# Optimization experiments

Hardware: AMD Instinct MI355X
Metric: run time of the kernel (lower is better)

The kernel has to match this reference:

```python
import jax, jax.numpy as jnp
import numpy as np

NX, NY, NC, NT = 320, 320, 20, 25


def ifft2c(x):
    # centered orthonormal 2D inverse FFT over axes (0,1)
    return jnp.fft.fftshift(
        jnp.fft.ifft2(jnp.fft.ifftshift(x, axes=(0, 1)), axes=(0, 1), norm='ortho'),
        axes=(0, 1))


def warp_bilinear(im, flw):
    # im: [Nx,Ny] complex, flw: [Nx,Ny,2] float pixel displacements
    # Sparse motion matrix application = bilinear gather at (x+u, y+v)
    Nx, Ny = im.shape
    gx, gy = jnp.meshgrid(jnp.arange(Nx, dtype=jnp.float32),
                          jnp.arange(Ny, dtype=jnp.float32), indexing='ij')
    xs = jnp.clip(gx + flw[..., 0], 0.0, Nx - 1.0)
    ys = jnp.clip(gy + flw[..., 1], 0.0, Ny - 1.0)
    x0 = jnp.floor(xs).astype(jnp.int32)
    y0 = jnp.floor(ys).astype(jnp.int32)
    x1 = jnp.minimum(x0 + 1, Nx - 1)
    y1 = jnp.minimum(y0 + 1, Ny - 1)
    wx = xs - x0.astype(jnp.float32)
    wy = ys - y0.astype(jnp.float32)
    return (im[x0, y0] * ((1 - wx) * (1 - wy))
            + im[x1, y0] * (wx * (1 - wy))
            + im[x0, y1] * ((1 - wx) * wy)
            + im[x1, y1] * (wx * wy))


def setup_inputs() -> dict:
    key = jax.random.key(0)
    ks = jax.random.split(key, 6)
    return {
        'kspace_re': jax.random.normal(ks[0], (NX, NY, NC), dtype=jnp.float32),
        'kspace_im': jax.random.normal(ks[1], (NX, NY, NC), dtype=jnp.float32),
        'mask': jax.random.uniform(ks[2], (NX, NY, NC, NT), dtype=jnp.float32),
        'smaps_re': jax.random.normal(ks[3], (NX, NY, NC), dtype=jnp.float32),
        'smaps_im': jax.random.normal(ks[4], (NX, NY, NC), dtype=jnp.float32),
        'flow': jax.random.normal(ks[5], (NX, NY, 2, NT), dtype=jnp.float32),
    }


def reference(kspace_re, kspace_im, mask, smaps_re, smaps_im, flow):
    kspace = kspace_re + 1j * kspace_im          # [Nx,Ny,Nc]
    smaps = smaps_re + 1j * smaps_im             # [Nx,Ny,Nc]
    # masked kspace for all motion states: [Nx,Ny,Nc,Nt]
    ksp_t = kspace[..., None] * mask.astype(kspace.dtype)
    coil_ims = ifft2c(ksp_t)                     # [Nx,Ny,Nc,Nt]
    # coil combine: sum_c ifft2c(k*m) * conj(smaps) -> [Nx,Ny,Nt]
    im_t = jnp.sum(coil_ims * jnp.conj(smaps)[..., None], axis=2)
    # per-frame sparse motion warp, then sum over motion states
    warped = jax.vmap(warp_bilinear, in_axes=(2, 3))(im_t, flow)  # [Nt,Nx,Ny]
    out = jnp.sum(warped, axis=0)                # [Nx,Ny] complex
    return jnp.stack([out.real, out.imag])       # [2,Nx,Ny] float32 view
```

## Files before the change

### kernel.cpp

```cpp
#include <hip/hip_runtime.h>
#include <hip/hip_fp16.h>
#include <math.h>

#define NXY 320
#define NC 20
#define NT 25
#define NPIX 102400
#define PI_F 3.14159265358979f
#define TWOPI_F 6.28318530717959f

__device__ __forceinline__ float2 cmul(float2 a, float2 b) {
    return make_float2(a.x * b.x - a.y * b.y, a.x * b.y + a.y * b.x);
}

struct Tw {
    float2 st[6];
    float  sgn[6];
    float2 w5[5];
    int J;
};

__device__ __forceinline__ void tw_init(Tw& t) {
    const int lane = threadIdx.x & 63;
    #pragma unroll
    for (int s = 0; s < 6; ++s) {
        const int h = 32 >> s;
        const bool up = (lane & h) != 0;
        t.sgn[s] = up ? -1.0f : 1.0f;
        if (up) {
            float ss, cc;
            __sincosf(PI_F * (float)(lane & (h - 1)) / (float)h, &ss, &cc);
            t.st[s] = make_float2(cc, ss);
        } else {
            t.st[s] = make_float2(1.0f, 0.0f);
        }
    }
    t.J = (int)(__brev((unsigned)lane) >> 26);
    t.w5[0] = make_float2(1.0f, 0.0f);
    #pragma unroll
    for (int r = 1; r < 5; ++r) {
        float ss, cc;
        __sincosf(TWOPI_F * (float)(r * t.J) / 320.0f, &ss, &cc);
        t.w5[r] = make_float2(cc, ss);
    }
}

__device__ __forceinline__ void fft320(const Tw& t, float2 x[5], float2 out[5]) {
    #pragma unroll
    for (int s = 0; s < 6; ++s) {
        const int h = 32 >> s;
        #pragma unroll
        for (int r = 0; r < 5; ++r) {
            float ox = __shfl_xor(x[r].x, h);
            float oy = __shfl_xor(x[r].y, h);
            float dx = fmaf(t.sgn[s], x[r].x, ox);
            float dy = fmaf(t.sgn[s], x[r].y, oy);
            x[r].x = dx * t.st[s].x - dy * t.st[s].y;
            x[r].y = dx * t.st[s].y + dy * t.st[s].x;
        }
    }
    float2 T[5];
    T[0] = x[0];
    #pragma unroll
    for (int r = 1; r < 5; ++r) T[r] = cmul(x[r], t.w5[r]);
    const float W5x[5] = {1.0f, 0.309016994f, -0.809016994f, -0.809016994f, 0.309016994f};
    const float W5y[5] = {0.0f, 0.951056516f, 0.587785252f, -0.587785252f, -0.951056516f};
    #pragma unroll
    for (int s5 = 0; s5 < 5; ++s5) {
        float2 acc = T[0];
        #pragma unroll
        for (int r = 1; r < 5; ++r) {
            const int k = (r * s5) % 5;
            acc.x += T[r].x * W5x[k] - T[r].y * W5y[k];
            acc.y += T[r].x * W5y[k] + T[r].y * W5x[k];
        }
        out[s5] = acc;
    }
}

__global__ __launch_bounds__(256) void k_prep_smaps(const float* __restrict__ smr,
                                                    const float* __restrict__ smi,
                                                    float2* __restrict__ smapsC) {
    const int p0 = blockIdx.x * 64;
    __shared__ float s_r[64 * 21];
    __shared__ float s_i[64 * 21];
    for (int j = threadIdx.x; j < 64 * NC; j += blockDim.x) {
        int p = j / NC, c = j - p * NC;
        s_r[p * 21 + c] = smr[(size_t)p0 * NC + j];
        s_i[p * 21 + c] = smi[(size_t)p0 * NC + j];
    }
    __syncthreads();
    for (int j = threadIdx.x; j < 64 * NC; j += blockDim.x) {
        int c = j >> 6, p = j & 63;
        int pg = p0 + p;
        int m = pg / NXY, n = pg - m * NXY;
        float sgn = (((m + n) & 1) ? -1.0f : 1.0f) * (1.0f / 320.0f);
        smapsC[(size_t)c * NPIX + pg] = make_float2(s_r[p * 21 + c] * sgn,
                                                    -s_i[p * 21 + c] * sgn);
    }
}

__global__ __launch_bounds__(256) void k_perm_smaps(const float2* __restrict__ smapsC,
                                                    __half2* __restrict__ smapsP) {
    const int c = blockIdx.x;
    const int s5 = blockIdx.y;
    const int v0 = blockIdx.z * 64;
    __shared__ __half2 t2[64 * 65];
    for (int j = threadIdx.x; j < 64 * 64; j += blockDim.x) {
        int ur = j >> 6, vc = j & 63;
        float2 v = smapsC[(size_t)c * NPIX + (size_t)(s5 * 64 + ur) * NXY + v0 + vc];
        t2[ur * 65 + vc] = __floats2half2_rn(v.x, v.y);
    }
    __syncthreads();
    for (int j = threadIdx.x; j < 64 * 64; j += blockDim.x) {
        int vr = j >> 6, lane = j & 63;
        int J = (int)(__brev((unsigned)lane) >> 26);
        smapsP[(size_t)((c * NXY + v0 + vr) * 5 + s5) * 64 + lane] = t2[J * 65 + vr];
    }
}

__global__ __launch_bounds__(256) void k_prep_input(const float* __restrict__ ksr,
                                                    const float* __restrict__ ksi,
                                                    const float* __restrict__ mask,
                                                    __half2* __restrict__ X0,
                                                    int t0, int G) {
    const int Q = NC * G;
    const int QP = Q + 1;
    const int p0 = blockIdx.x * 16;
    __shared__ float s_mask[16 * 501];
    __shared__ float s_kr[16 * 21];
    __shared__ float s_ki[16 * 21];
    for (int j = threadIdx.x; j < 16 * NC; j += blockDim.x) {
        int p = j / NC, c = j - p * NC;
        s_kr[p * 21 + c] = ksr[(size_t)p0 * NC + j];
        s_ki[p * 21 + c] = ksi[(size_t)p0 * NC + j];
    }
    for (int j = threadIdx.x; j < 16 * Q; j += blockDim.x) {
        int p = j / Q, qq = j - p * Q;
        int c = qq / G, tc = qq - c * G;
        s_mask[p * QP + qq] =
            mask[(size_t)(p0 + p) * (NC * NT) + c * NT + (t0 + tc)];
    }
    __syncthreads();
    for (int j = threadIdx.x; j < 16 * Q; j += blockDim.x) {
        int p = j & 15, q = j >> 4;
        int c = q / G;
        int pg = p0 + p;
        int m = pg / NXY, n = pg - m * NXY;
        float sgn = ((m + n) & 1) ? -1.0f : 1.0f;
        float mk = s_mask[p * QP + q] * sgn;
        X0[(size_t)q * NPIX + pg] =
            __floats2half2_rn(s_kr[p * 21 + c] * mk, s_ki[p * 21 + c] * mk);
    }
}

__global__ __launch_bounds__(256) void k_fft_rows(const __half2* __restrict__ X0,
                                                  __half2* __restrict__ Z, int G) {
    const int mtile = blockIdx.x;
    const int tc = blockIdx.y;
    const int c = blockIdx.z;
    const int q = c * G + tc;
    const int wave = threadIdx.x >> 6;
    const int lane = threadIdx.x & 63;
    const int m0 = mtile * 16;
    __shared__ __half2 tile[NXY * 17];
    Tw t;
    tw_init(t);
    const __half2* src = X0 + (size_t)q * NPIX;
    #pragma unroll
    for (int rnd = 0; rnd < 4; ++rnd) {
        int mm = rnd * 4 + wave;
        const __half2* row = src + (size_t)(m0 + mm) * NXY + lane * 5;
        float2 x[5], out[5];
        #pragma unroll
        for (int r = 0; r < 5; ++r) x[r] = __half22float2(row[r]);
        fft320(t, x, out);
        #pragma unroll
        for (int s5 = 0; s5 < 5; ++s5) {
            int v = t.J + 64 * s5;
            tile[v * 17 + mm] = __floats2half2_rn(out[s5].x, out[s5].y);
        }
    }
    __syncthreads();
    __half2* dst = Z + (size_t)q * NPIX + m0;
    for (int j = threadIdx.x; j < NXY * 16; j += blockDim.x) {
        int mm = j & 15, v = j >> 4;
        dst[(size_t)v * NXY + mm] = tile[v * 17 + mm];
    }
}

__global__ __launch_bounds__(256) void k_fft_cols_combine(const __half2* __restrict__ Z,
                                                          const __half2* __restrict__ smapsP,
                                                          float2* __restrict__ imt,
                                                          int t0, int G) {
    const int vtile = blockIdx.x;
    const int tc = blockIdx.y;
    const int wave = threadIdx.x >> 6;
    const int lane = threadIdx.x & 63;
    const int v0 = vtile * 8;
    __shared__ float tile_x[NXY * 9];
    __shared__ float tile_y[NXY * 9];
    Tw t;
    tw_init(t);
    float2 accA[5], accB[5];
    #pragma unroll
    for (int s5 = 0; s5 < 5; ++s5) {
        accA[s5] = make_float2(0.f, 0.f);
        accB[s5] = make_float2(0.f, 0.f);
    }
    const int vA = v0 + wave;
    const int vB = v0 + 4 + wave;
    for (int c = 0; c < NC; ++c) {
        const __half2* zc = Z + (size_t)(c * G + tc) * NPIX;
        {
            const __half2* col = zc + (size_t)vA * NXY + lane * 5;
            float2 x[5], out[5];
            #pragma unroll
            for (int r = 0; r < 5; ++r) x[r] = __half22float2(col[r]);
            fft320(t, x, out);
            const __half2* sp = smapsP + (size_t)((c * NXY + vA) * 5) * 64 + lane;
            #pragma unroll
            for (int s5 = 0; s5 < 5; ++s5) {
                float2 sm = __half22float2(sp[s5 * 64]);
                float2 tt = cmul(out[s5], sm);
                accA[s5].x += tt.x;
                accA[s5].y += tt.y;
            }
        }
        {
            const __half2* col = zc + (size_t)vB * NXY + lane * 5;
            float2 x[5], out[5];
            #pragma unroll
            for (int r = 0; r < 5; ++r) x[r] = __half22float2(col[r]);
            fft320(t, x, out);
            const __half2* sp = smapsP + (size_t)((c * NXY + vB) * 5) * 64 + lane;
            #pragma unroll
            for (int s5 = 0; s5 < 5; ++s5) {
                float2 sm = __half22float2(sp[s5 * 64]);
                float2 tt = cmul(out[s5], sm);
                accB[s5].x += tt.x;
                accB[s5].y += tt.y;
            }
        }
    }
    #pragma unroll
    for (int s5 = 0; s5 < 5; ++s5) {
        int u = t.J + 64 * s5;
        tile_x[u * 9 + wave] = accA[s5].x;
        tile_y[u * 9 + wave] = accA[s5].y;
        tile_x[u * 9 + 4 + wave] = accB[s5].x;
        tile_y[u * 9 + 4 + wave] = accB[s5].y;
    }
    __syncthreads();
    float2* dst = imt + (size_t)(t0 + tc) * NPIX + v0;
    for (int j = threadIdx.x; j < NXY * 8; j += blockDim.x) {
        int vv = j & 7, u = j >> 3;
        dst[(size_t)u * NXY + vv] = make_float2(tile_x[u * 9 + vv], tile_y[u * 9 + vv]);
    }
}

__global__ __launch_bounds__(256) void k_warp_sum(const float2* __restrict__ imt,
                                                  const float* __restrict__ flow,
                                                  float* __restrict__ out) {
    int p = blockIdx.x * blockDim.x + threadIdx.x;
    if (p >= NPIX) return;
    int x = p / NXY, y = p - x * NXY;
    float fx = (float)x, fy = (float)y;
    float ar = 0.f, ai = 0.f;
    const float* fl = flow + (size_t)p * (2 * NT);
    for (int t = 0; t < NT; ++t) {
        float u = fl[t];
        float v = fl[NT + t];
        float xs = fminf(fmaxf(fx + u, 0.0f), 319.0f);
        float ys = fminf(fmaxf(fy + v, 0.0f), 319.0f);
        float x0f = floorf(xs), y0f = floorf(ys);
        int x0 = (int)x0f, y0 = (int)y0f;
        int x1 = min(x0 + 1, NXY - 1), y1 = min(y0 + 1, NXY - 1);
        float wx = xs - x0f, wy = ys - y0f;
        const float2* base = imt + (size_t)t * NPIX;
        float2 c00 = base[x0 * NXY + y0];
        float2 c01 = base[x0 * NXY + y1];
        float2 c10 = base[x1 * NXY + y0];
        float2 c11 = base[x1 * NXY + y1];
        float w00 = (1.f - wx) * (1.f - wy), w01 = (1.f - wx) * wy;
        float w10 = wx * (1.f - wy), w11 = wx * wy;
        ar += c00.x * w00 + c01.x * w01 + c10.x * w10 + c11.x * w11;
        ai += c00.y * w00 + c01.y * w01 + c10.y * w10 + c11.y * w11;
    }
    out[p] = ar;
    out[NPIX + p] = ai;
}

extern "C" void kernel_launch(void* const* d_in, const int* in_sizes, int n_in,
                              void* d_out, int out_size, void* d_ws, size_t ws_size,
                              hipStream_t stream) {
    const float* ksr = (const float*)d_in[0];
    const float* ksi = (const float*)d_in[1];
    const float* mask = (const float*)d_in[2];
    const float* smr = (const float*)d_in[3];
    const float* smi = (const float*)d_in[4];
    const float* flow = (const float*)d_in[5];
    float* out = (float*)d_out;

    char* ws = (char*)d_ws;
    const size_t smapsC_bytes = (size_t)NC * NPIX * sizeof(float2);
    const size_t smapsP_bytes = (size_t)NC * NPIX * 5 * 64 / NXY * sizeof(__half2);
    const size_t imt_bytes = (size_t)NT * NPIX * sizeof(float2);
    const size_t fixed = smapsC_bytes + smapsP_bytes + imt_bytes;
    const size_t per_t = (size_t)2 * NC * NPIX * sizeof(__half2);

    int G = 1;
    if (ws_size > fixed + per_t) {
        size_t g = (ws_size - fixed) / per_t;
        G = (int)(g > (size_t)NT ? (size_t)NT : g);
    }
    if (G < 1) G = 1;

    float2* smapsC = (float2*)ws;
    __half2* smapsP = (__half2*)(ws + smapsC_bytes);
    float2* imt = (float2*)(ws + smapsC_bytes + smapsP_bytes);
    __half2* X0 = (__half2*)(ws + fixed);
    __half2* Z = (__half2*)(ws + fixed + (size_t)NC * G * NPIX * sizeof(__half2));

    k_prep_smaps<<<NPIX / 64, 256, 0, stream>>>(smr, smi, smapsC);
    k_perm_smaps<<<dim3(NC, 5, 5), 256, 0, stream>>>(smapsC, smapsP);
    for (int t0 = 0; t0 < NT; t0 += G) {
        int g = (NT - t0) < G ? (NT - t0) : G;
        k_prep_input<<<NPIX / 16, 256, 0, stream>>>(ksr, ksi, mask, X0, t0, g);
        k_fft_rows<<<dim3(20, g, NC), 256, 0, stream>>>(X0, Z, g);
        k_fft_cols_combine<<<dim3(40, g), 256, 0, stream>>>(Z, smapsP, imt, t0, g);
    }
    k_warp_sum<<<(NPIX + 255) / 256, 256, 0, stream>>>(imt, flow, out);
}
```

Baseline: 902.3 us.

## Batch FFTs per wave, split coil sum across blocks, stage flow in LDS

Several changes at once. The FFT routine is templated to process K independent transforms together, so the row and column passes interleave shuffles for ILP. The column/coil-combine kernel is split into two coil halves along a new grid dimension, doubling parallelism, and each half writes its partial image in fp16. The warp kernel then sums the two partials during its gathers. Mask loading in prep_input is made contiguous, and the warp kernel stages flow through LDS with coalesced loads. The trade-offs are extra gather traffic for the two partial images, fp16 precision loss on the intermediate images, and higher register pressure from batched FFTs.

```diff
diff --git a/kernel.cpp b/kernel.cpp
--- a/kernel.cpp
+++ b/kernel.cpp
@@ -45,36 +45,43 @@
     }
 }
 
-__device__ __forceinline__ void fft320(const Tw& t, float2 x[5], float2 out[5]) {
+template <int K>
+__device__ __forceinline__ void fft320xK(const Tw& t, float2 (&x)[K][5], float2 (&out)[K][5]) {
     #pragma unroll
     for (int s = 0; s < 6; ++s) {
         const int h = 32 >> s;
         #pragma unroll
         for (int r = 0; r < 5; ++r) {
-            float ox = __shfl_xor(x[r].x, h);
-            float oy = __shfl_xor(x[r].y, h);
-            float dx = fmaf(t.sgn[s], x[r].x, ox);
-            float dy = fmaf(t.sgn[s], x[r].y, oy);
-            x[r].x = dx * t.st[s].x - dy * t.st[s].y;
-            x[r].y = dx * t.st[s].y + dy * t.st[s].x;
-        }
-    }
-    float2 T[5];
-    T[0] = x[0];
-    #pragma unroll
-    for (int r = 1; r < 5; ++r) T[r] = cmul(x[r], t.w5[r]);
+            #pragma unroll
+            for (int k = 0; k < K; ++k) {
+                float ox = __shfl_xor(x[k][r].x, h);
+                float oy = __shfl_xor(x[k][r].y, h);
+                float dx = fmaf(t.sgn[s], x[k][r].x, ox);
+                float dy = fmaf(t.sgn[s], x[k][r].y, oy);
+                x[k][r].x = dx * t.st[s].x - dy * t.st[s].y;
+                x[k][r].y = dx * t.st[s].y + dy * t.st[s].x;
+            }
+        }
+    }
     const float W5x[5] = {1.0f, 0.309016994f, -0.809016994f, -0.809016994f, 0.309016994f};
     const float W5y[5] = {0.0f, 0.951056516f, 0.587785252f, -0.587785252f, -0.951056516f};
     #pragma unroll
-    for (int s5 = 0; s5 < 5; ++s5) {
-        float2 acc = T[0];
-        #pragma unroll
-        for (int r = 1; r < 5; ++r) {
-            const int k = (r * s5) % 5;
-            acc.x += T[r].x * W5x[k] - T[r].y * W5y[k];
-            acc.y += T[r].x * W5y[k] + T[r].y * W5x[k];
-        }
-        out[s5] = acc;
+    for (int k = 0; k < K; ++k) {
+        float2 T[5];
+        T[0] = x[k][0];
+        #pragma unroll
+        for (int r = 1; r < 5; ++r) T[r] = cmul(x[k][r], t.w5[r]);
+        #pragma unroll
+        for (int s5 = 0; s5 < 5; ++s5) {
+            float2 acc = T[0];
+            #pragma unroll
+            for (int r = 1; r < 5; ++r) {
+                const int kk = (r * s5) % 5;
+                acc.x += T[r].x * W5x[kk] - T[r].y * W5y[kk];
+                acc.y += T[r].x * W5y[kk] + T[r].y * W5x[kk];
+            }
+            out[k][s5] = acc;
+        }
     }
 }
 
@@ -124,8 +131,6 @@
                                                     const float* __restrict__ mask,
                                                     __half2* __restrict__ X0,
                                                     int t0, int G) {
-    const int Q = NC * G;
-    const int QP = Q + 1;
     const int p0 = blockIdx.x * 16;
     __shared__ float s_mask[16 * 501];
     __shared__ float s_kr[16 * 21];
@@ -135,22 +140,26 @@
         s_kr[p * 21 + c] = ksr[(size_t)p0 * NC + j];
         s_ki[p * 21 + c] = ksi[(size_t)p0 * NC + j];
     }
-    for (int j = threadIdx.x; j < 16 * Q; j += blockDim.x) {
-        int p = j / Q, qq = j - p * Q;
-        int c = qq / G, tc = qq - c * G;
-        s_mask[p * QP + qq] =
-            mask[(size_t)(p0 + p) * (NC * NT) + c * NT + (t0 + tc)];
-    }
-    __syncthreads();
-    for (int j = threadIdx.x; j < 16 * Q; j += blockDim.x) {
-        int p = j & 15, q = j >> 4;
-        int c = q / G;
-        int pg = p0 + p;
-        int m = pg / NXY, n = pg - m * NXY;
-        float sgn = ((m + n) & 1) ? -1.0f : 1.0f;
-        float mk = s_mask[p * QP + q] * sgn;
-        X0[(size_t)q * NPIX + pg] =
-            __floats2half2_rn(s_kr[p * 21 + c] * mk, s_ki[p * 21 + c] * mk);
+    for (int j = threadIdx.x; j < 16 * 500; j += blockDim.x) {
+        int p = j / 500, col = j - p * 500;
+        s_mask[p * 501 + col] = mask[(size_t)p0 * 500 + j];
+    }
+    __syncthreads();
+    const int p = threadIdx.x & 15;
+    const int g16 = threadIdx.x >> 4;
+    const int pg = p0 + p;
+    const int m = pg / NXY;
+    const int n = pg - m * NXY;
+    const float sgn = ((m + n) & 1) ? -1.0f : 1.0f;
+    #pragma unroll
+    for (int c = 0; c < NC; ++c) {
+        const float kr = s_kr[p * 21 + c] * sgn;
+        const float ki = s_ki[p * 21 + c] * sgn;
+        for (int tc = g16; tc < G; tc += 16) {
+            const int q = c * G + tc;
+            const float mk = s_mask[p * 501 + c * NT + t0 + tc];
+            X0[(size_t)q * NPIX + pg] = __floats2half2_rn(kr * mk, ki * mk);
+        }
     }
 }
 
@@ -167,18 +176,21 @@
     Tw t;
     tw_init(t);
     const __half2* src = X0 + (size_t)q * NPIX;
-    #pragma unroll
-    for (int rnd = 0; rnd < 4; ++rnd) {
-        int mm = rnd * 4 + wave;
-        const __half2* row = src + (size_t)(m0 + mm) * NXY + lane * 5;
-        float2 x[5], out[5];
-        #pragma unroll
-        for (int r = 0; r < 5; ++r) x[r] = __half22float2(row[r]);
-        fft320(t, x, out);
+    float2 x[4][5], out[4][5];
+    #pragma unroll
+    for (int k = 0; k < 4; ++k) {
+        const __half2* row = src + (size_t)(m0 + wave + 4 * k) * NXY + lane * 5;
+        #pragma unroll
+        for (int r = 0; r < 5; ++r) x[k][r] = __half22float2(row[r]);
+    }
+    fft320xK<4>(t, x, out);
+    #pragma unroll
+    for (int k = 0; k < 4; ++k) {
+        const int mm = wave + 4 * k;
         #pragma unroll
         for (int s5 = 0; s5 < 5; ++s5) {
             int v = t.J + 64 * s5;
-            tile[v * 17 + mm] = __floats2half2_rn(out[s5].x, out[s5].y);
+            tile[v * 17 + mm] = __floats2half2_rn(out[k][s5].x, out[k][s5].y);
         }
     }
     __syncthreads();
@@ -191,97 +203,99 @@
 
 __global__ __launch_bounds__(256) void k_fft_cols_combine(const __half2* __restrict__ Z,
                                                           const __half2* __restrict__ smapsP,
-                                                          float2* __restrict__ imt,
+                                                          __half2* __restrict__ imtP,
                                                           int t0, int G) {
     const int vtile = blockIdx.x;
     const int tc = blockIdx.y;
+    const int half = blockIdx.z;
     const int wave = threadIdx.x >> 6;
     const int lane = threadIdx.x & 63;
     const int v0 = vtile * 8;
-    __shared__ float tile_x[NXY * 9];
-    __shared__ float tile_y[NXY * 9];
+    const int vA = v0 + wave;
+    const int vB = v0 + 4 + wave;
+    __shared__ __half2 tile[NXY * 9];
     Tw t;
     tw_init(t);
-    float2 accA[5], accB[5];
-    #pragma unroll
-    for (int s5 = 0; s5 < 5; ++s5) {
-        accA[s5] = make_float2(0.f, 0.f);
-        accB[s5] = make_float2(0.f, 0.f);
-    }
-    const int vA = v0 + wave;
-    const int vB = v0 + 4 + wave;
-    for (int c = 0; c < NC; ++c) {
+    float2 acc[2][5];
+    #pragma unroll
+    for (int k = 0; k < 2; ++k)
+        #pragma unroll
+        for (int s5 = 0; s5 < 5; ++s5) acc[k][s5] = make_float2(0.f, 0.f);
+    const int c0 = half * 10;
+    for (int c = c0; c < c0 + 10; ++c) {
         const __half2* zc = Z + (size_t)(c * G + tc) * NPIX;
-        {
-            const __half2* col = zc + (size_t)vA * NXY + lane * 5;
-            float2 x[5], out[5];
-            #pragma unroll
-            for (int r = 0; r < 5; ++r) x[r] = __half22float2(col[r]);
-            fft320(t, x, out);
-            const __half2* sp = smapsP + (size_t)((c * NXY + vA) * 5) * 64 + lane;
-            #pragma unroll
-            for (int s5 = 0; s5 < 5; ++s5) {
-                float2 sm = __half22float2(sp[s5 * 64]);
-                float2 tt = cmul(out[s5], sm);
-                accA[s5].x += tt.x;
-                accA[s5].y += tt.y;
-            }
-        }
-        {
-            const __half2* col = zc + (size_t)vB * NXY + lane * 5;
-            float2 x[5], out[5];
-            #pragma unroll
-            for (int r = 0; r < 5; ++r) x[r] = __half22float2(col[r]);
-            fft320(t, x, out);
-            const __half2* sp = smapsP + (size_t)((c * NXY + vB) * 5) * 64 + lane;
-            #pragma unroll
-            for (int s5 = 0; s5 < 5; ++s5) {
-                float2 sm = __half22float2(sp[s5 * 64]);
-                float2 tt = cmul(out[s5], sm);
-                accB[s5].x += tt.x;
-                accB[s5].y += tt.y;
-            }
+        float2 x[2][5], out[2][5];
+        const __half2* colA = zc + (size_t)vA * NXY + lane * 5;
+        const __half2* colB = zc + (size_t)vB * NXY + lane * 5;
+        #pragma unroll
+        for (int r = 0; r < 5; ++r) {
+            x[0][r] = __half22float2(colA[r]);
+            x[1][r] = __half22float2(colB[r]);
+        }
+        fft320xK<2>(t, x, out);
+        const __half2* spA = smapsP + (size_t)((c * NXY + vA) * 5) * 64 + lane;
+        const __half2* spB = smapsP + (size_t)((c * NXY + vB) * 5) * 64 + lane;
+        #pragma unroll
+        for (int s5 = 0; s5 < 5; ++s5) {
+            float2 smA = __half22float2(spA[s5 * 64]);
+            float2 smB = __half22float2(spB[s5 * 64]);
+            float2 ta = cmul(out[0][s5], smA);
+            float2 tb = cmul(out[1][s5], smB);
+            acc[0][s5].x += ta.x; acc[0][s5].y += ta.y;
+            acc[1][s5].x += tb.x; acc[1][s5].y += tb.y;
         }
     }
     #pragma unroll
     for (int s5 = 0; s5 < 5; ++s5) {
         int u = t.J + 64 * s5;
-        tile_x[u * 9 + wave] = accA[s5].x;
-        tile_y[u * 9 + wave] = accA[s5].y;
-        tile_x[u * 9 + 4 + wave] = accB[s5].x;
-        tile_y[u * 9 + 4 + wave] = accB[s5].y;
-    }
-    __syncthreads();
-    float2* dst = imt + (size_t)(t0 + tc) * NPIX + v0;
+        tile[u * 9 + wave] = __floats2half2_rn(acc[0][s5].x, acc[0][s5].y);
+        tile[u * 9 + 4 + wave] = __floats2half2_rn(acc[1][s5].x, acc[1][s5].y);
+    }
+    __syncthreads();
+    __half2* dst = imtP + (size_t)(half * NT + t0 + tc) * NPIX + v0;
     for (int j = threadIdx.x; j < NXY * 8; j += blockDim.x) {
         int vv = j & 7, u = j >> 3;
-        dst[(size_t)u * NXY + vv] = make_float2(tile_x[u * 9 + vv], tile_y[u * 9 + vv]);
-    }
-}
-
-__global__ __launch_bounds__(256) void k_warp_sum(const float2* __restrict__ imt,
+        dst[(size_t)u * NXY + vv] = tile[u * 9 + vv];
+    }
+}
+
+__global__ __launch_bounds__(256) void k_warp_sum(const __half2* __restrict__ imtP,
                                                   const float* __restrict__ flow,
                                                   float* __restrict__ out) {
-    int p = blockIdx.x * blockDim.x + threadIdx.x;
-    if (p >= NPIX) return;
-    int x = p / NXY, y = p - x * NXY;
-    float fx = (float)x, fy = (float)y;
+    const int p0 = blockIdx.x * 256;
+    const int tid = threadIdx.x;
+    __shared__ float s_fl[2 * NT * 257];
+    for (int j = tid; j < 256 * 50; j += 256) {
+        int pp = j / 50, rem = j - pp * 50;
+        int d = rem / 25, tt = rem - d * 25;
+        s_fl[(d * NT + tt) * 257 + pp] = flow[(size_t)p0 * 50 + j];
+    }
+    __syncthreads();
+    const int p = p0 + tid;
+    const int x = p / NXY, y = p - x * NXY;
+    const float fx = (float)x, fy = (float)y;
     float ar = 0.f, ai = 0.f;
-    const float* fl = flow + (size_t)p * (2 * NT);
     for (int t = 0; t < NT; ++t) {
-        float u = fl[t];
-        float v = fl[NT + t];
+        float u = s_fl[t * 257 + tid];
+        float v = s_fl[(NT + t) * 257 + tid];
         float xs = fminf(fmaxf(fx + u, 0.0f), 319.0f);
         float ys = fminf(fmaxf(fy + v, 0.0f), 319.0f);
         float x0f = floorf(xs), y0f = floorf(ys);
         int x0 = (int)x0f, y0 = (int)y0f;
         int x1 = min(x0 + 1, NXY - 1), y1 = min(y0 + 1, NXY - 1);
         float wx = xs - x0f, wy = ys - y0f;
-        const float2* base = imt + (size_t)t * NPIX;
-        float2 c00 = base[x0 * NXY + y0];
-        float2 c01 = base[x0 * NXY + y1];
-        float2 c10 = base[x1 * NXY + y0];
-        float2 c11 = base[x1 * NXY + y1];
+        const __half2* b0 = imtP + (size_t)t * NPIX;
+        const __half2* b1 = imtP + (size_t)(NT + t) * NPIX;
+        int i00 = x0 * NXY + y0, i01 = x0 * NXY + y1;
+        int i10 = x1 * NXY + y0, i11 = x1 * NXY + y1;
+        float2 c00 = __half22float2(b0[i00]); float2 d00 = __half22float2(b1[i00]);
+        float2 c01 = __half22float2(b0[i01]); float2 d01 = __half22float2(b1[i01]);
+        float2 c10 = __half22float2(b0[i10]); float2 d10 = __half22float2(b1[i10]);
+        float2 c11 = __half22float2(b0[i11]); float2 d11 = __half22float2(b1[i11]);
+        c00.x += d00.x; c00.y += d00.y;
+        c01.x += d01.x; c01.y += d01.y;
+        c10.x += d10.x; c10.y += d10.y;
+        c11.x += d11.x; c11.y += d11.y;
         float w00 = (1.f - wx) * (1.f - wy), w01 = (1.f - wx) * wy;
         float w10 = wx * (1.f - wy), w11 = wx * wy;
         ar += c00.x * w00 + c01.x * w01 + c10.x * w10 + c11.x * w11;
@@ -304,9 +318,9 @@
 
     char* ws = (char*)d_ws;
     const size_t smapsC_bytes = (size_t)NC * NPIX * sizeof(float2);
-    const size_t smapsP_bytes = (size_t)NC * NPIX * 5 * 64 / NXY * sizeof(__half2);
-    const size_t imt_bytes = (size_t)NT * NPIX * sizeof(float2);
-    const size_t fixed = smapsC_bytes + smapsP_bytes + imt_bytes;
+    const size_t smapsP_bytes = (size_t)NC * NPIX * sizeof(__half2);
+    const size_t imtP_bytes = (size_t)2 * NT * NPIX * sizeof(__half2);
+    const size_t fixed = smapsC_bytes + smapsP_bytes + imtP_bytes;
     const size_t per_t = (size_t)2 * NC * NPIX * sizeof(__half2);
 
     int G = 1;
@@ -318,7 +332,7 @@
 
     float2* smapsC = (float2*)ws;
     __half2* smapsP = (__half2*)(ws + smapsC_bytes);
-    float2* imt = (float2*)(ws + smapsC_bytes + smapsP_bytes);
+    __half2* imtP = (__half2*)(ws + smapsC_bytes + smapsP_bytes);
     __half2* X0 = (__half2*)(ws + fixed);
     __half2* Z = (__half2*)(ws + fixed + (size_t)NC * G * NPIX * sizeof(__half2));
 
@@ -328,7 +342,7 @@
         int g = (NT - t0) < G ? (NT - t0) : G;
         k_prep_input<<<NPIX / 16, 256, 0, stream>>>(ksr, ksi, mask, X0, t0, g);
         k_fft_rows<<<dim3(20, g, NC), 256, 0, stream>>>(X0, Z, g);
-        k_fft_cols_combine<<<dim3(40, g), 256, 0, stream>>>(Z, smapsP, imt, t0, g);
-    }
-    k_warp_sum<<<(NPIX + 255) / 256, 256, 0, stream>>>(imt, flow, out);
-}
+        k_fft_cols_combine<<<dim3(40, g, 2), 256, 0, stream>>>(Z, smapsP, imtP, t0, g);
+    }
+    k_warp_sum<<<NPIX / 256, 256, 0, stream>>>(imtP, flow, out);
+}
```

Measured after the change: 823.6 us. 1.1x faster.
